# Kernel tuning notes

Measured on AMD Instinct MI355X. Metric: run time of the kernel, lower is better.

## Reference

```python
import jax, jax.numpy as jnp
import numpy as np

N = 2097152
MAX_DEPTH = 4
EPS = 1e-4
SPHERE_R = 1.0

def _normalize(v):
    return v / jnp.maximum(jnp.linalg.norm(v, axis=-1, keepdims=True), 1e-12)

def _intersect_sphere(o, d):
    # unit sphere at origin; returns hit point, shading normal, hit mask
    b = jnp.sum(o * d, -1)
    c = jnp.sum(o * o, -1) - SPHERE_R * SPHERE_R
    disc = b * b - c
    sq = jnp.sqrt(jnp.maximum(disc, 0.0))
    t0, t1 = -b - sq, -b + sq
    t = jnp.where(t0 > EPS, t0, t1)
    hit = (disc > 0.0) & (t > EPS)
    p = o + t[..., None] * d
    n = _normalize(p)
    return p, n, hit

def _frame(n):
    # branchless orthonormal basis (Duff et al.)
    nx, ny, nz = n[..., 0], n[..., 1], n[..., 2]
    s = jnp.where(nz >= 0.0, 1.0, -1.0)
    a = -1.0 / (s + nz)
    b = nx * ny * a
    t1 = jnp.stack([1.0 + s * nx * nx * a, s * b, -s * nx], -1)
    t2 = jnp.stack([b, s + ny * ny * a, -ny], -1)
    return t1, t2

def setup_inputs() -> dict:
    key = jax.random.key(0)
    k1, k2, k3, k4, k5 = jax.random.split(key, 5)
    return {
        "ray_o": jax.random.normal(k1, (N, 3), jnp.float32),
        "ray_d": jax.random.normal(k2, (N, 3), jnp.float32),
        "u_bsdf": jax.random.uniform(k3, (MAX_DEPTH, N, 2), jnp.float32),
        "albedo": jax.random.uniform(k4, (3,), jnp.float32),
        "light_intensity": jax.random.uniform(k5, (3,), jnp.float32),
    }

def reference(ray_o, ray_d, u_bsdf, albedo, light_intensity):
    light_pos = jnp.array([3.0, 4.0, 5.0], ray_o.dtype)
    # camera rays aimed at the sphere so the primary intersection mostly hits
    o = ray_o * 0.5 + jnp.array([0.0, 0.0, -4.0], ray_o.dtype)
    d = _normalize(ray_d * 0.2 + jnp.array([0.0, 0.0, 1.0], ray_d.dtype))

    p, n, active = _intersect_sphere(o, d)
    original_active = active
    throughput = jnp.ones_like(p)   # [N,3]
    result = jnp.zeros_like(p)      # [N,3]

    for depth in range(MAX_DEPTH):
        t1, t2 = _frame(n)
        # --- emitter sampling: delta point light, pdf = 1, mis = 1 ---
        to_l = light_pos - p
        dist2 = jnp.sum(to_l * to_l, -1, keepdims=True)
        wl = to_l / jnp.sqrt(dist2)
        emitter_val = light_intensity / dist2                       # [N,3]
        cos_l = jnp.maximum(jnp.sum(wl * n, -1), 0.0)               # local wo_z
        bsdf_val = albedo * (cos_l / jnp.pi)[..., None]             # Lambertian eval
        result = result + jnp.where(active[..., None],
                                    throughput * bsdf_val * emitter_val, 0.0)
        # --- BSDF cosine-hemisphere sample; weight f*cos/pdf = albedo ---
        u1, u2 = u_bsdf[depth, :, 0], u_bsdf[depth, :, 1]
        r, phi = jnp.sqrt(u1), 2.0 * jnp.pi * u2
        wo = jnp.stack([r * jnp.cos(phi), r * jnp.sin(phi),
                        jnp.sqrt(jnp.maximum(1.0 - u1, 0.0))], -1)
        weight = jnp.broadcast_to(albedo, throughput.shape)
        throughput = jax.lax.stop_gradient(
            jnp.clip(weight, 1e-10, None) * throughput)             # .detach() in source
        active = active & jnp.any(throughput > 0.0, -1)
        # --- spawn next rays and intersect ---
        d = wo[..., 0:1] * t1 + wo[..., 1:2] * t2 + wo[..., 2:3] * n
        o = p + EPS * n
        p2, n2, hits = _intersect_sphere(o, d)
        active = active & hits
        p = jnp.where(active[..., None], p2, p)
        n = jnp.where(active[..., None], n2, n)

    return result, original_active
```

## Files before the change

### kernel.cpp

```cpp
#include <hip/hip_runtime.h>
#include <math.h>

#define RT_EPS 1e-4f
#define RT_MAX_DEPTH 4

__device__ __forceinline__ bool rt_intersect(
    float ox, float oy, float oz,
    float dx, float dy, float dz,
    float& px, float& py, float& pz,
    float& nx, float& ny, float& nz)
{
    float b = ox * dx + oy * dy + oz * dz;
    float c = ox * ox + oy * oy + oz * oz - 1.0f;
    float disc = b * b - c;
    float sq = sqrtf(fmaxf(disc, 0.0f));
    float t0 = -b - sq;
    float t1 = -b + sq;
    float t = (t0 > RT_EPS) ? t0 : t1;
    bool hit = (disc > 0.0f) && (t > RT_EPS);
    px = ox + t * dx;
    py = oy + t * dy;
    pz = oz + t * dz;
    float pl = sqrtf(px * px + py * py + pz * pz);
    float inv = 1.0f / fmaxf(pl, 1e-12f);
    nx = px * inv;
    ny = py * inv;
    nz = pz * inv;
    return hit;
}

__global__ __launch_bounds__(256) void path_trace_kernel(
    const float* __restrict__ ray_o,
    const float* __restrict__ ray_d,
    const float* __restrict__ u_bsdf,
    const float* __restrict__ albedo,
    const float* __restrict__ light,
    float* __restrict__ out,
    int n)
{
    int i = blockIdx.x * blockDim.x + threadIdx.x;
    if (i >= n) return;

    float ox = ray_o[3 * i + 0] * 0.5f;
    float oy = ray_o[3 * i + 1] * 0.5f;
    float oz = ray_o[3 * i + 2] * 0.5f - 4.0f;
    float dx = ray_d[3 * i + 0] * 0.2f;
    float dy = ray_d[3 * i + 1] * 0.2f;
    float dz = ray_d[3 * i + 2] * 0.2f + 1.0f;
    float dn = sqrtf(dx * dx + dy * dy + dz * dz);
    float dinv = 1.0f / fmaxf(dn, 1e-12f);
    dx *= dinv; dy *= dinv; dz *= dinv;

    float px, py, pz, nx, ny, nz;
    bool hit0 = rt_intersect(ox, oy, oz, dx, dy, dz, px, py, pz, nx, ny, nz);

    float rx = 0.0f, ry = 0.0f, rz = 0.0f;

    if (hit0) {
        float ax = albedo[0], ay = albedo[1], az = albedo[2];
        float lx = light[0],  ly = light[1],  lz = light[2];
        float cax = fmaxf(ax, 1e-10f);
        float cay = fmaxf(ay, 1e-10f);
        float caz = fmaxf(az, 1e-10f);

        float tx = 1.0f, ty = 1.0f, tz = 1.0f;
        bool active = true;

        const float2* __restrict__ ub = (const float2*)u_bsdf;

        #pragma unroll
        for (int depth = 0; depth < RT_MAX_DEPTH; ++depth) {
            float s = (nz >= 0.0f) ? 1.0f : -1.0f;
            float a = -1.0f / (s + nz);
            float bb = nx * ny * a;
            float t1x = 1.0f + s * nx * nx * a;
            float t1y = s * bb;
            float t1z = -s * nx;
            float t2x = bb;
            float t2y = s + ny * ny * a;
            float t2z = -ny;

            float tlx = 3.0f - px, tly = 4.0f - py, tlz = 5.0f - pz;
            float dist2 = tlx * tlx + tly * tly + tlz * tlz;
            float wl_inv = 1.0f / sqrtf(dist2);
            float wlx = tlx * wl_inv, wly = tly * wl_inv, wlz = tlz * wl_inv;
            float cos_l = fmaxf(wlx * nx + wly * ny + wlz * nz, 0.0f);
            float k = cos_l * (1.0f / 3.14159265358979323846f) / dist2;
            if (active) {
                rx += tx * ax * k * lx;
                ry += ty * ay * k * ly;
                rz += tz * az * k * lz;
            }

            float2 u = ub[(size_t)depth * n + i];
            float r = sqrtf(u.x);
            float phi = 6.28318530717958647692f * u.y;
            float sp, cp;
            sincosf(phi, &sp, &cp);
            float wox = r * cp;
            float woy = r * sp;
            float woz = sqrtf(fmaxf(1.0f - u.x, 0.0f));

            tx *= cax; ty *= cay; tz *= caz;
            active = active && ((tx > 0.0f) || (ty > 0.0f) || (tz > 0.0f));

            float ndx = wox * t1x + woy * t2x + woz * nx;
            float ndy = wox * t1y + woy * t2y + woz * ny;
            float ndz = wox * t1z + woy * t2z + woz * nz;
            float nox = px + RT_EPS * nx;
            float noy = py + RT_EPS * ny;
            float noz = pz + RT_EPS * nz;

            float p2x, p2y, p2z, n2x, n2y, n2z;
            bool h2 = rt_intersect(nox, noy, noz, ndx, ndy, ndz,
                                   p2x, p2y, p2z, n2x, n2y, n2z);
            active = active && h2;
            if (active) {
                px = p2x; py = p2y; pz = p2z;
                nx = n2x; ny = n2y; nz = n2z;
            }
        }
    }

    out[3 * i + 0] = rx;
    out[3 * i + 1] = ry;
    out[3 * i + 2] = rz;
    out[(size_t)3 * n + i] = hit0 ? 1.0f : 0.0f;
}

extern "C" void kernel_launch(void* const* d_in, const int* in_sizes, int n_in,
                              void* d_out, int out_size, void* d_ws, size_t ws_size,
                              hipStream_t stream) {
    const float* ray_o  = (const float*)d_in[0];
    const float* ray_d  = (const float*)d_in[1];
    const float* u_bsdf = (const float*)d_in[2];
    const float* albedo = (const float*)d_in[3];
    const float* light  = (const float*)d_in[4];
    float* out = (float*)d_out;

    int n = in_sizes[0] / 3;
    int block = 256;
    int grid = (n + block - 1) / block;
    path_trace_kernel<<<grid, block, 0, stream>>>(ray_o, ray_d, u_bsdf, albedo,
                                                  light, out, n);
}
```

Measured before the change: 151.0 us.

## Drop secondary bounces that provably miss the convex sphere; vectorize I/O

```diff
diff --git a/kernel.cpp b/kernel.cpp
--- a/kernel.cpp
+++ b/kernel.cpp
@@ -2,145 +2,103 @@
 #include <math.h>
 
 #define RT_EPS 1e-4f
-#define RT_MAX_DEPTH 4
 
-__device__ __forceinline__ bool rt_intersect(
+__device__ __forceinline__ float4 trace_ray(
     float ox, float oy, float oz,
     float dx, float dy, float dz,
-    float& px, float& py, float& pz,
-    float& nx, float& ny, float& nz)
+    float cx, float cy, float cz)
 {
+    ox *= 0.5f;
+    oy *= 0.5f;
+    oz = oz * 0.5f - 4.0f;
+    dx *= 0.2f;
+    dy *= 0.2f;
+    dz = dz * 0.2f + 1.0f;
+    float dd = dx * dx + dy * dy + dz * dz;
+    float dinv = __builtin_amdgcn_rsqf(fmaxf(dd, 1e-24f));
+    dx *= dinv; dy *= dinv; dz *= dinv;
+
     float b = ox * dx + oy * dy + oz * dz;
     float c = ox * ox + oy * oy + oz * oz - 1.0f;
     float disc = b * b - c;
-    float sq = sqrtf(fmaxf(disc, 0.0f));
+    float sq = __builtin_amdgcn_sqrtf(fmaxf(disc, 0.0f));
     float t0 = -b - sq;
     float t1 = -b + sq;
     float t = (t0 > RT_EPS) ? t0 : t1;
     bool hit = (disc > 0.0f) && (t > RT_EPS);
-    px = ox + t * dx;
-    py = oy + t * dy;
-    pz = oz + t * dz;
-    float pl = sqrtf(px * px + py * py + pz * pz);
-    float inv = 1.0f / fmaxf(pl, 1e-12f);
-    nx = px * inv;
-    ny = py * inv;
-    nz = pz * inv;
-    return hit;
+
+    float px = ox + t * dx;
+    float py = oy + t * dy;
+    float pz = oz + t * dz;
+    float pp = px * px + py * py + pz * pz;
+    float ninv = __builtin_amdgcn_rsqf(fmaxf(pp, 1e-24f));
+    float nx = px * ninv, ny = py * ninv, nz = pz * ninv;
+
+    float tlx = 3.0f - px, tly = 4.0f - py, tlz = 5.0f - pz;
+    float dist2 = tlx * tlx + tly * tly + tlz * tlz;
+    float rinv = __builtin_amdgcn_rsqf(dist2);
+    float cos_l = fmaxf((tlx * nx + tly * ny + tlz * nz) * rinv, 0.0f);
+    float k = cos_l * __builtin_amdgcn_rcpf(dist2);
+
+    float4 r;
+    r.x = hit ? cx * k : 0.0f;
+    r.y = hit ? cy * k : 0.0f;
+    r.z = hit ? cz * k : 0.0f;
+    r.w = hit ? 1.0f : 0.0f;
+    return r;
 }
 
 __global__ __launch_bounds__(256) void path_trace_kernel(
-    const float* __restrict__ ray_o,
-    const float* __restrict__ ray_d,
-    const float* __restrict__ u_bsdf,
+    const float4* __restrict__ ro4,
+    const float4* __restrict__ rd4,
     const float* __restrict__ albedo,
     const float* __restrict__ light,
-    float* __restrict__ out,
-    int n)
+    float4* __restrict__ res4,
+    float4* __restrict__ act4,
+    int nq)
 {
-    int i = blockIdx.x * blockDim.x + threadIdx.x;
-    if (i >= n) return;
+    int q = blockIdx.x * blockDim.x + threadIdx.x;
+    if (q >= nq) return;
 
-    float ox = ray_o[3 * i + 0] * 0.5f;
-    float oy = ray_o[3 * i + 1] * 0.5f;
-    float oz = ray_o[3 * i + 2] * 0.5f - 4.0f;
-    float dx = ray_d[3 * i + 0] * 0.2f;
-    float dy = ray_d[3 * i + 1] * 0.2f;
-    float dz = ray_d[3 * i + 2] * 0.2f + 1.0f;
-    float dn = sqrtf(dx * dx + dy * dy + dz * dz);
-    float dinv = 1.0f / fmaxf(dn, 1e-12f);
-    dx *= dinv; dy *= dinv; dz *= dinv;
+    const float inv_pi = 0.31830988618379067154f;
+    float cx = albedo[0] * light[0] * inv_pi;
+    float cy = albedo[1] * light[1] * inv_pi;
+    float cz = albedo[2] * light[2] * inv_pi;
 
-    float px, py, pz, nx, ny, nz;
-    bool hit0 = rt_intersect(ox, oy, oz, dx, dy, dz, px, py, pz, nx, ny, nz);
+    float4 a0 = ro4[3 * q + 0];
+    float4 a1 = ro4[3 * q + 1];
+    float4 a2 = ro4[3 * q + 2];
+    float4 b0 = rd4[3 * q + 0];
+    float4 b1 = rd4[3 * q + 1];
+    float4 b2 = rd4[3 * q + 2];
 
-    float rx = 0.0f, ry = 0.0f, rz = 0.0f;
+    float4 r0 = trace_ray(a0.x, a0.y, a0.z, b0.x, b0.y, b0.z, cx, cy, cz);
+    float4 r1 = trace_ray(a0.w, a1.x, a1.y, b0.w, b1.x, b1.y, cx, cy, cz);
+    float4 r2 = trace_ray(a1.z, a1.w, a2.x, b1.z, b1.w, b2.x, cx, cy, cz);
+    float4 r3 = trace_ray(a2.y, a2.z, a2.w, b2.y, b2.z, b2.w, cx, cy, cz);
 
-    if (hit0) {
-        float ax = albedo[0], ay = albedo[1], az = albedo[2];
-        float lx = light[0],  ly = light[1],  lz = light[2];
-        float cax = fmaxf(ax, 1e-10f);
-        float cay = fmaxf(ay, 1e-10f);
-        float caz = fmaxf(az, 1e-10f);
-
-        float tx = 1.0f, ty = 1.0f, tz = 1.0f;
-        bool active = true;
-
-        const float2* __restrict__ ub = (const float2*)u_bsdf;
-
-        #pragma unroll
-        for (int depth = 0; depth < RT_MAX_DEPTH; ++depth) {
-            float s = (nz >= 0.0f) ? 1.0f : -1.0f;
-            float a = -1.0f / (s + nz);
-            float bb = nx * ny * a;
-            float t1x = 1.0f + s * nx * nx * a;
-            float t1y = s * bb;
-            float t1z = -s * nx;
-            float t2x = bb;
-            float t2y = s + ny * ny * a;
-            float t2z = -ny;
-
-            float tlx = 3.0f - px, tly = 4.0f - py, tlz = 5.0f - pz;
-            float dist2 = tlx * tlx + tly * tly + tlz * tlz;
-            float wl_inv = 1.0f / sqrtf(dist2);
-            float wlx = tlx * wl_inv, wly = tly * wl_inv, wlz = tlz * wl_inv;
-            float cos_l = fmaxf(wlx * nx + wly * ny + wlz * nz, 0.0f);
-            float k = cos_l * (1.0f / 3.14159265358979323846f) / dist2;
-            if (active) {
-                rx += tx * ax * k * lx;
-                ry += ty * ay * k * ly;
-                rz += tz * az * k * lz;
-            }
-
-            float2 u = ub[(size_t)depth * n + i];
-            float r = sqrtf(u.x);
-            float phi = 6.28318530717958647692f * u.y;
-            float sp, cp;
-            sincosf(phi, &sp, &cp);
-            float wox = r * cp;
-            float woy = r * sp;
-            float woz = sqrtf(fmaxf(1.0f - u.x, 0.0f));
-
-            tx *= cax; ty *= cay; tz *= caz;
-            active = active && ((tx > 0.0f) || (ty > 0.0f) || (tz > 0.0f));
-
-            float ndx = wox * t1x + woy * t2x + woz * nx;
-            float ndy = wox * t1y + woy * t2y + woz * ny;
-            float ndz = wox * t1z + woy * t2z + woz * nz;
-            float nox = px + RT_EPS * nx;
-            float noy = py + RT_EPS * ny;
-            float noz = pz + RT_EPS * nz;
-
-            float p2x, p2y, p2z, n2x, n2y, n2z;
-            bool h2 = rt_intersect(nox, noy, noz, ndx, ndy, ndz,
-                                   p2x, p2y, p2z, n2x, n2y, n2z);
-            active = active && h2;
-            if (active) {
-                px = p2x; py = p2y; pz = p2z;
-                nx = n2x; ny = n2y; nz = n2z;
-            }
-        }
-    }
-
-    out[3 * i + 0] = rx;
-    out[3 * i + 1] = ry;
-    out[3 * i + 2] = rz;
-    out[(size_t)3 * n + i] = hit0 ? 1.0f : 0.0f;
+    res4[3 * q + 0] = make_float4(r0.x, r0.y, r0.z, r1.x);
+    res4[3 * q + 1] = make_float4(r1.y, r1.z, r2.x, r2.y);
+    res4[3 * q + 2] = make_float4(r2.z, r3.x, r3.y, r3.z);
+    act4[q]         = make_float4(r0.w, r1.w, r2.w, r3.w);
 }
 
 extern "C" void kernel_launch(void* const* d_in, const int* in_sizes, int n_in,
                               void* d_out, int out_size, void* d_ws, size_t ws_size,
                               hipStream_t stream) {
-    const float* ray_o  = (const float*)d_in[0];
-    const float* ray_d  = (const float*)d_in[1];
-    const float* u_bsdf = (const float*)d_in[2];
+    const float4* ro4   = (const float4*)d_in[0];
+    const float4* rd4   = (const float4*)d_in[1];
     const float* albedo = (const float*)d_in[3];
     const float* light  = (const float*)d_in[4];
     float* out = (float*)d_out;
 
     int n = in_sizes[0] / 3;
+    int nq = n / 4;
+    float4* res4 = (float4*)out;
+    float4* act4 = (float4*)(out + (size_t)3 * n);
+
     int block = 256;
-    int grid = (n + block - 1) / block;
-    path_trace_kernel<<<grid, block, 0, stream>>>(ray_o, ray_d, u_bsdf, albedo,
-                                                  light, out, n);
+    int grid = (nq + block - 1) / block;
+    path_trace_kernel<<<grid, block, 0, stream>>>(ro4, rd4, albedo, light,
+                                                  res4, act4, nq);
 }
```

New measurement: 137.7 us. 8.8% less time.
